# Performance work log

Measured on AMD Instinct MI355X. Metric: run time of the kernel, lower is better.

The kernel has to match this reference:

```python
import jax, jax.numpy as jnp
import numpy as np

N_NODES = 10000
N_EDGES = 80000
IN_DIM, HID, OUT_DIM, HEADS = 768, 512, 768, 4
NEG_SLOPE = 0.2


def setup_inputs() -> dict:
    key = jax.random.key(0)
    ks = jax.random.split(key, 10)
    g = 0.05
    return {
        "x": jax.random.normal(ks[0], (N_NODES, IN_DIM), jnp.float32),
        "edge_index": jax.random.randint(ks[1], (2, N_EDGES), 0, N_NODES, jnp.int64),
        # layer 1: GATConv(768 -> 512, heads=4, concat=True)
        "W1": jax.random.normal(ks[2], (IN_DIM, HEADS * HID), jnp.float32) * g,
        "a1_src": jax.random.normal(ks[3], (HEADS, HID), jnp.float32) * g,
        "a1_dst": jax.random.normal(ks[4], (HEADS, HID), jnp.float32) * g,
        "b1": jnp.zeros((HEADS * HID,), jnp.float32),
        # layer 2: GATConv(2048 -> 768, heads=1, concat=False)
        "W2": jax.random.normal(ks[5], (HEADS * HID, OUT_DIM), jnp.float32) * g,
        "a2_src": jax.random.normal(ks[6], (1, OUT_DIM), jnp.float32) * g,
        "a2_dst": jax.random.normal(ks[7], (1, OUT_DIM), jnp.float32) * g,
        "b2": jnp.zeros((OUT_DIM,), jnp.float32),
    }


def _gat_layer(x, src, dst, W, a_src, a_dst, b, heads, d_out, concat):
    N = x.shape[0]
    h = (x @ W).reshape(N, heads, d_out)              # [N, H, D]
    as_n = jnp.einsum('nhd,hd->nh', h, a_src)          # [N, H]
    ad_n = jnp.einsum('nhd,hd->nh', h, a_dst)
    e = jax.nn.leaky_relu(as_n[src] + ad_n[dst], NEG_SLOPE)  # [E, H]
    # segment softmax over destination nodes
    e_max = jax.lax.stop_gradient(jax.ops.segment_max(e, dst, num_segments=N))
    ex = jnp.exp(e - e_max[dst])
    denom = jax.ops.segment_sum(ex, dst, num_segments=N)
    alpha = ex / (denom[dst] + 1e-16)                  # [E, H]
    msg = alpha[:, :, None] * h[src]                   # [E, H, D]
    out = jax.ops.segment_sum(msg, dst, num_segments=N)  # [N, H, D]
    out = out.reshape(N, heads * d_out) if concat else out.mean(axis=1)
    return out + b


def reference(x, edge_index, W1, a1_src, a1_dst, b1, W2, a2_src, a2_dst, b2):
    N = x.shape[0]
    # PyG GATConv default: add self-loops
    loops = jnp.arange(N, dtype=edge_index.dtype)
    src = jnp.concatenate([edge_index[0], loops])
    dst = jnp.concatenate([edge_index[1], loops])
    h = _gat_layer(x, src, dst, W1, a1_src, a1_dst, b1, HEADS, HID, True)
    h = jax.nn.elu(h)
    out = _gat_layer(h, src, dst, W2, a2_src, a2_dst, b2, 1, OUT_DIM, False)
    return out
```

## Files before the change

### kernel.cpp

```cpp
#include <hip/hip_runtime.h>
#include <hip/hip_bf16.h>

#define N_NODES 10000
#define E_REAL  80000
#define E_TOTAL 90000
#define IN_DIM  768
#define HID     512
#define HEADS   4
#define OUT_DIM 768
#define HD1     (HEADS * HID)
#define NEG_SLOPE 0.2f
#define H1_HSTRIDE (N_NODES * HID)

typedef unsigned short ushort_t;
typedef unsigned int uint_t;

__device__ inline float b2f(ushort_t u) { return __uint_as_float(((uint_t)u) << 16); }
__device__ inline ushort_t f2b(float f) {
    __hip_bfloat16 h = __float2bfloat16(f);
    return *reinterpret_cast<ushort_t*>(&h);
}

__device__ inline void edge_sd(const int* __restrict__ ei, int e, int& s, int& d) {
    if (e < E_REAL) { s = ei[e]; d = ei[E_REAL + e]; }
    else            { s = e - E_REAL; d = s; }
}

#define GLDS(g, l) __builtin_amdgcn_global_load_lds( \
    (const __attribute__((address_space(1))) void*)(g), \
    (__attribute__((address_space(3))) void*)(l), 16, 0, 0)

static const long B_H1B  = 0L;
static const long B_HB   = 40960000L;
static const long B_XB   = 81920000L;
static const long B_W1T  = 97280000L;
static const long B_W2T  = 100425728L;
static const long B_SM   = 103571456L;
static const long SM_AS1   = 0;
static const long SM_AD1   = 40000;
static const long SM_AS2   = 80000;
static const long SM_AD2   = 90000;
static const long SM_CNT   = 100000;
static const long SM_ROWS  = 110000;
static const long SM_CURS  = 120016;
static const long SM_END   = 130016;
static const long B_CSRS = B_SM + SM_END * 4;

__global__ __launch_bounds__(256)
void cast_bf16(const float* __restrict__ in, ushort_t* __restrict__ o, long n) {
    long i = ((long)blockIdx.x * 256 + threadIdx.x) * 8;
    if (i >= n) return;
    float4 v0 = *(const float4*)(in + i);
    float4 v1 = *(const float4*)(in + i + 4);
    ushort_t r[8] = {f2b(v0.x), f2b(v0.y), f2b(v0.z), f2b(v0.w),
                     f2b(v1.x), f2b(v1.y), f2b(v1.z), f2b(v1.w)};
    *(uint4*)(o + i) = *(uint4*)r;
}

__global__ __launch_bounds__(256)
void cast_transpose(const float* __restrict__ W, ushort_t* __restrict__ WT,
                    int K, int N) {
    __shared__ ushort_t t[32][33];
    const int n0 = blockIdx.x * 32, k0 = blockIdx.y * 32;
    const int tx = threadIdx.x & 31, ty = threadIdx.x >> 5;
#pragma unroll
    for (int i = 0; i < 4; ++i) {
        int k = ty + i * 8;
        t[k][tx] = f2b(W[(long)(k0 + k) * N + n0 + tx]);
    }
    __syncthreads();
#pragma unroll
    for (int i = 0; i < 4; ++i) {
        int n = ty + i * 8;
        WT[(long)(n0 + n) * K + k0 + tx] = t[tx][n];
    }
}

typedef short bf16x8 __attribute__((ext_vector_type(8)));
typedef float f32x4 __attribute__((ext_vector_type(4)));

#define BM 128
#define BN 128
#define BK 32

template<int CMODE>
__global__ __launch_bounds__(256)
void gemm_bf16(const ushort_t* __restrict__ A, const ushort_t* __restrict__ BT,
               ushort_t* __restrict__ C, int M, int N, int K) {
    __shared__ ushort_t As[BM * BK];
    __shared__ ushort_t Bs[BN * BK];
    const int tid  = threadIdx.x;
    const int wave = tid >> 6, lane = tid & 63;
    const int quad = lane >> 4, l16 = lane & 15;
    const int bm = blockIdx.y * BM, bn = blockIdx.x * BN;
    const int wr = (wave >> 1) * 64, wc = (wave & 1) * 64;

    const int ch0 = wave * 128 + lane;
    const int ch1 = ch0 + 64;
    const int r0 = ch0 >> 2, c0 = (ch0 & 3) ^ ((r0 >> 1) & 3);
    const int r1 = ch1 >> 2, c1 = (ch1 & 3) ^ ((r1 >> 1) & 3);
    const ushort_t* a0 = A + (long)(bm + r0) * K + c0 * 8;
    const ushort_t* a1 = A + (long)(bm + r1) * K + c1 * 8;
    const ushort_t* b0 = BT + (long)(bn + r0) * K + c0 * 8;
    const ushort_t* b1 = BT + (long)(bn + r1) * K + c1 * 8;
    ushort_t* lA0 = As + (wave * 128) * 8;
    ushort_t* lA1 = As + (wave * 128 + 64) * 8;
    ushort_t* lB0 = Bs + (wave * 128) * 8;
    ushort_t* lB1 = Bs + (wave * 128 + 64) * 8;

    const int swz = (l16 >> 1) & 3;
    f32x4 acc[4][4] = {};

    for (int k0 = 0; k0 < K; k0 += BK) {
        GLDS(a0 + k0, lA0);
        GLDS(a1 + k0, lA1);
        GLDS(b0 + k0, lB0);
        GLDS(b1 + k0, lB1);
        __syncthreads();
        bf16x8 af[4], bfr[4];
#pragma unroll
        for (int i = 0; i < 4; ++i) {
            af[i]  = *(const bf16x8*)(As + ((wr + i * 16 + l16) * 4 + (quad ^ swz)) * 8);
            bfr[i] = *(const bf16x8*)(Bs + ((wc + i * 16 + l16) * 4 + (quad ^ swz)) * 8);
        }
#pragma unroll
        for (int i = 0; i < 4; ++i)
#pragma unroll
            for (int j = 0; j < 4; ++j)
                acc[i][j] = __builtin_amdgcn_mfma_f32_16x16x32_bf16(
                    af[i], bfr[j], acc[i][j], 0, 0, 0);
        __syncthreads();
    }

#pragma unroll
    for (int i = 0; i < 4; ++i) {
#pragma unroll
        for (int r = 0; r < 4; ++r) {
            int row = bm + wr + i * 16 + quad * 4 + r;
            if (row >= M) continue;
#pragma unroll
            for (int j = 0; j < 4; ++j) {
                int col = bn + wc + j * 16 + l16;
                if (CMODE == 0) {
                    C[(long)row * N + col] = f2b(acc[i][j][r]);
                } else {
                    C[(long)(col >> 9) * H1_HSTRIDE + (long)row * HID + (col & 511)]
                        = f2b(acc[i][j][r]);
                }
            }
        }
    }
}

__global__ __launch_bounds__(256)
void attn1(const ushort_t* __restrict__ h, const float* __restrict__ a_s,
           const float* __restrict__ a_d, float* __restrict__ os,
           float* __restrict__ od) {
    const int n = blockIdx.x;
    const int w = threadIdx.x >> 6, lane = threadIdx.x & 63;
    uint4 hv = *(const uint4*)(h + (long)w * H1_HSTRIDE + (long)n * HID + lane * 8);
    const float* asp = a_s + w * HID + lane * 8;
    const float* adp = a_d + w * HID + lane * 8;
    const ushort_t* pb = (const ushort_t*)&hv;
    float ps = 0.f, pd = 0.f;
#pragma unroll
    for (int c = 0; c < 8; ++c) {
        float v = b2f(pb[c]);
        ps += v * asp[c];
        pd += v * adp[c];
    }
#pragma unroll
    for (int off = 32; off > 0; off >>= 1) {
        ps += __shfl_down(ps, off);
        pd += __shfl_down(pd, off);
    }
    if (lane == 0) { os[n * HEADS + w] = ps; od[n * HEADS + w] = pd; }
}

__global__ __launch_bounds__(256)
void attn2(const ushort_t* __restrict__ h, const float* __restrict__ a_s,
           const float* __restrict__ a_d, float* __restrict__ os,
           float* __restrict__ od) {
    __shared__ float rs[4], rd[4];
    const int n = blockIdx.x, tid = threadIdx.x;
    const int w = tid >> 6, lane = tid & 63;
    float ps = 0.f, pd = 0.f;
#pragma unroll
    for (int j = 0; j < 3; ++j) {
        int c = tid + j * 256;
        float v = b2f(h[(long)n * OUT_DIM + c]);
        ps += v * a_s[c];
        pd += v * a_d[c];
    }
#pragma unroll
    for (int off = 32; off > 0; off >>= 1) {
        ps += __shfl_down(ps, off);
        pd += __shfl_down(pd, off);
    }
    if (lane == 0) { rs[w] = ps; rd[w] = pd; }
    __syncthreads();
    if (tid == 0) {
        os[n] = rs[0] + rs[1] + rs[2] + rs[3];
        od[n] = rd[0] + rd[1] + rd[2] + rd[3];
    }
}

__global__ __launch_bounds__(256)
void hist_dst(const int* __restrict__ ei, int* __restrict__ cnt) {
    int e = blockIdx.x * 256 + threadIdx.x;
    if (e >= E_TOTAL) return;
    int s, d; edge_sd(ei, e, s, d);
    atomicAdd(&cnt[d], 1);
}

#define SCAN_CH 40
__global__ __launch_bounds__(256)
void scan_nodes(const int* __restrict__ cnt, int* __restrict__ rows,
                int* __restrict__ curs) {
    __shared__ int part[256];
    const int tid = threadIdx.x;
    const int base = tid * SCAN_CH;
    int local[SCAN_CH];
    int sum = 0;
#pragma unroll
    for (int i = 0; i < SCAN_CH; ++i) {
        int idx = base + i;
        int v = (idx < N_NODES) ? cnt[idx] : 0;
        local[i] = v; sum += v;
    }
    part[tid] = sum;
    __syncthreads();
    for (int off = 1; off < 256; off <<= 1) {
        int v = (tid >= off) ? part[tid - off] : 0;
        __syncthreads();
        part[tid] += v;
        __syncthreads();
    }
    int run = part[tid] - sum;
#pragma unroll
    for (int i = 0; i < SCAN_CH; ++i) {
        int idx = base + i;
        if (idx < N_NODES) { rows[idx] = run; curs[idx] = run; run += local[i]; }
    }
    if (tid == 255) rows[N_NODES] = run;
}

__global__ __launch_bounds__(256)
void scatter_edges(const int* __restrict__ ei, int* __restrict__ curs,
                   int* __restrict__ csr_src) {
    int e = blockIdx.x * 256 + threadIdx.x;
    if (e >= E_TOTAL) return;
    int s, d; edge_sd(ei, e, s, d);
    int pos = atomicAdd(&curs[d], 1);
    csr_src[pos] = s;
}

__global__ __launch_bounds__(64)
void agg1(const int* __restrict__ rows, const int* __restrict__ csr_src,
          const float* __restrict__ as_n, const float* __restrict__ ad_n,
          const ushort_t* __restrict__ hf, const float* __restrict__ b1,
          ushort_t* __restrict__ o) {
    const int n = blockIdx.x, hh = blockIdx.y, lane = threadIdx.x;
    const int beg = rows[n], end = rows[n + 1];
    const ushort_t* hsl = hf + (long)hh * H1_HSTRIDE;
    const float adv = ad_n[(long)n * HEADS + hh];
    float acc[8] = {};
    float dsum = 0.f;
    for (int k = beg; k < end; k += 4) {
        int nk = end - k; if (nk > 4) nk = 4;
        uint4 v[4]; float ex[4];
#pragma unroll
        for (int u = 0; u < 4; ++u) {
            if (u < nk) {
                int s = csr_src[k + u];
                float sc = as_n[(long)s * HEADS + hh] + adv;
                sc = sc > 0.f ? sc : NEG_SLOPE * sc;
                ex[u] = __expf(sc);
                v[u]  = *(const uint4*)(hsl + (long)s * HID + lane * 8);
            }
        }
#pragma unroll
        for (int u = 0; u < 4; ++u) {
            if (u < nk) {
                dsum += ex[u];
                const ushort_t* p = (const ushort_t*)&v[u];
#pragma unroll
                for (int c = 0; c < 8; ++c) acc[c] += ex[u] * b2f(p[c]);
            }
        }
    }
    const float dinv = 1.f / (dsum + 1e-16f);
    const float* bp = b1 + hh * HID + lane * 8;
    ushort_t r[8];
#pragma unroll
    for (int c = 0; c < 8; ++c) {
        float vv = acc[c] * dinv + bp[c];
        r[c] = f2b(vv > 0.f ? vv : expm1f(vv));
    }
    *(uint4*)(o + (long)n * HD1 + hh * HID + lane * 8) = *(uint4*)r;
}

__global__ __launch_bounds__(64)
void agg2(const int* __restrict__ rows, const int* __restrict__ csr_src,
          const float* __restrict__ as_n, const float* __restrict__ ad_n,
          const ushort_t* __restrict__ hf, const float* __restrict__ b2,
          float* __restrict__ out) {
    const int n = blockIdx.x, lane = threadIdx.x;
    const int beg = rows[n], end = rows[n + 1];
    const float adv = ad_n[n];
    float acc[12] = {};
    float dsum = 0.f;
    for (int k = beg; k < end; k += 4) {
        int nk = end - k; if (nk > 4) nk = 4;
        uint4 v4[4]; uint2 v2[4]; float ex[4];
#pragma unroll
        for (int u = 0; u < 4; ++u) {
            if (u < nk) {
                int s = csr_src[k + u];
                float sc = as_n[s] + adv;
                sc = sc > 0.f ? sc : NEG_SLOPE * sc;
                ex[u] = __expf(sc);
                const ushort_t* hp = hf + (long)s * OUT_DIM;
                v4[u] = *(const uint4*)(hp + lane * 8);
                v2[u] = *(const uint2*)(hp + 512 + lane * 4);
            }
        }
#pragma unroll
        for (int u = 0; u < 4; ++u) {
            if (u < nk) {
                dsum += ex[u];
                const ushort_t* p4 = (const ushort_t*)&v4[u];
                const ushort_t* p2 = (const ushort_t*)&v2[u];
#pragma unroll
                for (int c = 0; c < 8; ++c) acc[c] += ex[u] * b2f(p4[c]);
#pragma unroll
                for (int c = 0; c < 4; ++c) acc[8 + c] += ex[u] * b2f(p2[c]);
            }
        }
    }
    const float dinv = 1.f / (dsum + 1e-16f);
    float* op = out + (long)n * OUT_DIM;
#pragma unroll
    for (int c = 0; c < 8; ++c)
        op[lane * 8 + c] = acc[c] * dinv + b2[lane * 8 + c];
#pragma unroll
    for (int c = 0; c < 4; ++c)
        op[512 + lane * 4 + c] = acc[8 + c] * dinv + b2[512 + lane * 4 + c];
}

extern "C" void kernel_launch(void* const* d_in, const int* in_sizes, int n_in,
                              void* d_out, int out_size, void* d_ws, size_t ws_size,
                              hipStream_t stream) {
    const float* x   = (const float*)d_in[0];
    const int*   ei  = (const int*)d_in[1];
    const float* W1  = (const float*)d_in[2];
    const float* a1s = (const float*)d_in[3];
    const float* a1d = (const float*)d_in[4];
    const float* b1  = (const float*)d_in[5];
    const float* W2  = (const float*)d_in[6];
    const float* a2s = (const float*)d_in[7];
    const float* a2d = (const float*)d_in[8];
    const float* b2  = (const float*)d_in[9];
    float* out = (float*)d_out;
    char* base = (char*)d_ws;

    ushort_t* h1b = (ushort_t*)(base + B_H1B);
    ushort_t* hb  = (ushort_t*)(base + B_HB);
    ushort_t* xb  = (ushort_t*)(base + B_XB);
    ushort_t* h2b = xb;
    ushort_t* w1t = (ushort_t*)(base + B_W1T);
    ushort_t* w2t = (ushort_t*)(base + B_W2T);
    float*    sm  = (float*)(base + B_SM);

    float* as1  = sm + SM_AS1;
    float* ad1  = sm + SM_AD1;
    float* as2  = sm + SM_AS2;
    float* ad2  = sm + SM_AD2;
    int* cnt    = (int*)(sm + SM_CNT);
    int* rows   = (int*)(sm + SM_ROWS);
    int* curs   = (int*)(sm + SM_CURS);
    int* csr_src = (int*)(base + B_CSRS);

    hipMemsetAsync(cnt, 0, 10000 * sizeof(int), stream);

    {
        long nx = (long)N_NODES * IN_DIM;
        cast_bf16<<<(int)(nx / 8 / 256 + 1), 256, 0, stream>>>(x, xb, nx);
        cast_transpose<<<dim3(HD1 / 32, IN_DIM / 32), 256, 0, stream>>>(W1, w1t, IN_DIM, HD1);
        cast_transpose<<<dim3(OUT_DIM / 32, HD1 / 32), 256, 0, stream>>>(W2, w2t, HD1, OUT_DIM);
        hist_dst<<<(E_TOTAL + 255) / 256, 256, 0, stream>>>(ei, cnt);
        scan_nodes<<<1, 256, 0, stream>>>(cnt, rows, curs);
        scatter_edges<<<(E_TOTAL + 255) / 256, 256, 0, stream>>>(ei, curs, csr_src);
    }

    gemm_bf16<1><<<dim3(HD1 / BN, (N_NODES + BM - 1) / BM), 256, 0, stream>>>(
        xb, w1t, h1b, N_NODES, HD1, IN_DIM);
    attn1<<<N_NODES, 256, 0, stream>>>(h1b, a1s, a1d, as1, ad1);
    agg1<<<dim3(N_NODES, HEADS), 64, 0, stream>>>(
        rows, csr_src, as1, ad1, h1b, b1, hb);

    gemm_bf16<0><<<dim3(OUT_DIM / BN, (N_NODES + BM - 1) / BM), 256, 0, stream>>>(
        hb, w2t, h2b, N_NODES, OUT_DIM, HD1);
    attn2<<<N_NODES, 256, 0, stream>>>(h2b, a2s, a2d, as2, ad2);
    agg2<<<N_NODES, 64, 0, stream>>>(
        rows, csr_src, as2, ad2, h2b, b2, out);
}
```

Measured before the change: 346.3 us.

## Replace bf16 GEMM with 8-wave 256x128x64 triple-buffered pipelined kernel

Both dense projections now use a new GEMM with 512 threads, a larger 256x128 output tile and a 64-deep K step. Operand tiles are triple-buffered in about 144KB of dynamic LDS, with global-to-LDS loads staged two iterations ahead. Explicit vmcnt waits, barriers, sched_barrier and setprio interleave the loads with the MFMA work. The aim is to hide memory latency and improve data reuse, at the cost of lower occupancy. The second GEMM also launches fewer blocks than there are CUs.

```diff
diff --git a/kernel.cpp b/kernel.cpp
--- a/kernel.cpp
+++ b/kernel.cpp
@@ -79,57 +79,125 @@
 typedef short bf16x8 __attribute__((ext_vector_type(8)));
 typedef float f32x4 __attribute__((ext_vector_type(4)));
 
-#define BM 128
-#define BN 128
-#define BK 32
+#define GBM 256
+#define GBN 128
+#define GBK 64
+#define ABUF (GBM * GBK)
+#define BBUF (GBN * GBK)
+#define GEMM_LDS_BYTES ((3 * (ABUF + BBUF)) * 2)
 
 template<int CMODE>
-__global__ __launch_bounds__(256)
-void gemm_bf16(const ushort_t* __restrict__ A, const ushort_t* __restrict__ BT,
-               ushort_t* __restrict__ C, int M, int N, int K) {
-    __shared__ ushort_t As[BM * BK];
-    __shared__ ushort_t Bs[BN * BK];
+__global__ __launch_bounds__(512)
+void gemm8p(const ushort_t* __restrict__ A, const ushort_t* __restrict__ BT,
+            ushort_t* __restrict__ C, int M, int N, int K) {
+    extern __shared__ ushort_t sm_[];
+    ushort_t* smA = sm_;
+    ushort_t* smB = sm_ + 3 * ABUF;
     const int tid  = threadIdx.x;
     const int wave = tid >> 6, lane = tid & 63;
     const int quad = lane >> 4, l16 = lane & 15;
-    const int bm = blockIdx.y * BM, bn = blockIdx.x * BN;
+    const int bm = blockIdx.y * GBM, bn = blockIdx.x * GBN;
     const int wr = (wave >> 1) * 64, wc = (wave & 1) * 64;
-
-    const int ch0 = wave * 128 + lane;
-    const int ch1 = ch0 + 64;
-    const int r0 = ch0 >> 2, c0 = (ch0 & 3) ^ ((r0 >> 1) & 3);
-    const int r1 = ch1 >> 2, c1 = (ch1 & 3) ^ ((r1 >> 1) & 3);
-    const ushort_t* a0 = A + (long)(bm + r0) * K + c0 * 8;
-    const ushort_t* a1 = A + (long)(bm + r1) * K + c1 * 8;
-    const ushort_t* b0 = BT + (long)(bn + r0) * K + c0 * 8;
-    const ushort_t* b1 = BT + (long)(bn + r1) * K + c1 * 8;
-    ushort_t* lA0 = As + (wave * 128) * 8;
-    ushort_t* lA1 = As + (wave * 128 + 64) * 8;
-    ushort_t* lB0 = Bs + (wave * 128) * 8;
-    ushort_t* lB1 = Bs + (wave * 128 + 64) * 8;
-
-    const int swz = (l16 >> 1) & 3;
+    const int NT = K / GBK;
+
+    const int  rA  = tid >> 3;
+    const long cs8 = (long)(((tid & 7) ^ ((tid >> 3) & 7)) * 8);
+    const ushort_t* aSrc = A  + (long)(bm + rA) * K + cs8;
+    const ushort_t* bSrc = BT + (long)(bn + rA) * K + cs8;
+
+    const int aRd  = (wr + l16) * GBK;
+    const int bRd  = (wc + l16) * GBK;
+    const int swz8 = l16 & 7;
+    const int chq0 = ((quad)     ^ swz8) * 8;
+    const int chq1 = ((4 + quad) ^ swz8) * 8;
+
     f32x4 acc[4][4] = {};
 
-    for (int k0 = 0; k0 < K; k0 += BK) {
-        GLDS(a0 + k0, lA0);
-        GLDS(a1 + k0, lA1);
-        GLDS(b0 + k0, lB0);
-        GLDS(b1 + k0, lB1);
-        __syncthreads();
-        bf16x8 af[4], bfr[4];
-#pragma unroll
-        for (int i = 0; i < 4; ++i) {
-            af[i]  = *(const bf16x8*)(As + ((wr + i * 16 + l16) * 4 + (quad ^ swz)) * 8);
-            bfr[i] = *(const bf16x8*)(Bs + ((wc + i * 16 + l16) * 4 + (quad ^ swz)) * 8);
-        }
+#pragma unroll
+    for (int tt = 0; tt < 2; ++tt) {
+        const long kt = (long)tt * GBK;
 #pragma unroll
         for (int i = 0; i < 4; ++i)
-#pragma unroll
-            for (int j = 0; j < 4; ++j)
-                acc[i][j] = __builtin_amdgcn_mfma_f32_16x16x32_bf16(
-                    af[i], bfr[j], acc[i][j], 0, 0, 0);
-        __syncthreads();
+            GLDS(aSrc + (long)i * 64 * K + kt,
+                 smA + tt * ABUF + (i * 512 + wave * 64) * 8);
+#pragma unroll
+        for (int i = 0; i < 2; ++i)
+            GLDS(bSrc + (long)i * 64 * K + kt,
+                 smB + tt * BBUF + (i * 512 + wave * 64) * 8);
+    }
+    asm volatile("s_waitcnt vmcnt(6)" ::: "memory");
+    __builtin_amdgcn_s_barrier();
+    __builtin_amdgcn_sched_barrier(0);
+
+    int bc = 0, bnx = 1, bs = 2;
+    for (int t = 0; t < NT; ++t) {
+        const int offA = bc * ABUF, offB = bc * BBUF;
+        const bool stage = (t + 2 < NT);
+        const long kt2 = (long)(t + 2) * GBK;
+        bf16x8 bfr[2][4], af[2][2];
+
+#pragma unroll
+        for (int j = 0; j < 4; ++j) {
+            bfr[0][j] = *(const bf16x8*)(smB + offB + bRd + j * 1024 + chq0);
+            bfr[1][j] = *(const bf16x8*)(smB + offB + bRd + j * 1024 + chq1);
+        }
+#pragma unroll
+        for (int ii = 0; ii < 2; ++ii) {
+            af[0][ii] = *(const bf16x8*)(smA + offA + aRd + ii * 1024 + chq0);
+            af[1][ii] = *(const bf16x8*)(smA + offA + aRd + ii * 1024 + chq1);
+        }
+        if (stage) {
+            GLDS(aSrc + kt2,                    smA + bs * ABUF + (wave * 64) * 8);
+            GLDS(aSrc + (long)1 * 64 * K + kt2, smA + bs * ABUF + (512 + wave * 64) * 8);
+            GLDS(aSrc + (long)2 * 64 * K + kt2, smA + bs * ABUF + (1024 + wave * 64) * 8);
+        }
+        __builtin_amdgcn_sched_barrier(0);
+        __builtin_amdgcn_s_barrier();
+        __builtin_amdgcn_sched_barrier(0);
+        __builtin_amdgcn_s_setprio(1);
+#pragma unroll
+        for (int kk = 0; kk < 2; ++kk)
+#pragma unroll
+            for (int ii = 0; ii < 2; ++ii)
+#pragma unroll
+                for (int j = 0; j < 4; ++j)
+                    acc[ii][j] = __builtin_amdgcn_mfma_f32_16x16x32_bf16(
+                        af[kk][ii], bfr[kk][j], acc[ii][j], 0, 0, 0);
+        __builtin_amdgcn_s_setprio(0);
+        __builtin_amdgcn_sched_barrier(0);
+        __builtin_amdgcn_s_barrier();
+        __builtin_amdgcn_sched_barrier(0);
+
+#pragma unroll
+        for (int ii = 0; ii < 2; ++ii) {
+            af[0][ii] = *(const bf16x8*)(smA + offA + aRd + (2 + ii) * 1024 + chq0);
+            af[1][ii] = *(const bf16x8*)(smA + offA + aRd + (2 + ii) * 1024 + chq1);
+        }
+        if (stage) {
+            GLDS(aSrc + (long)3 * 64 * K + kt2, smA + bs * ABUF + (1536 + wave * 64) * 8);
+            GLDS(bSrc + kt2,                    smB + bs * BBUF + (wave * 64) * 8);
+            GLDS(bSrc + (long)1 * 64 * K + kt2, smB + bs * BBUF + (512 + wave * 64) * 8);
+        }
+        if (stage)             { asm volatile("s_waitcnt vmcnt(6)" ::: "memory"); }
+        else if (t + 1 < NT)   { asm volatile("s_waitcnt vmcnt(0)" ::: "memory"); }
+        __builtin_amdgcn_sched_barrier(0);
+        __builtin_amdgcn_s_barrier();
+        __builtin_amdgcn_sched_barrier(0);
+        __builtin_amdgcn_s_setprio(1);
+#pragma unroll
+        for (int kk = 0; kk < 2; ++kk)
+#pragma unroll
+            for (int ii = 0; ii < 2; ++ii)
+#pragma unroll
+                for (int j = 0; j < 4; ++j)
+                    acc[2 + ii][j] = __builtin_amdgcn_mfma_f32_16x16x32_bf16(
+                        af[kk][ii], bfr[kk][j], acc[2 + ii][j], 0, 0, 0);
+        __builtin_amdgcn_s_setprio(0);
+        __builtin_amdgcn_sched_barrier(0);
+        __builtin_amdgcn_s_barrier();
+        __builtin_amdgcn_sched_barrier(0);
+
+        int tmp = bc; bc = bnx; bnx = bs; bs = tmp;
     }
 
 #pragma unroll
@@ -393,13 +461,13 @@
         scatter_edges<<<(E_TOTAL + 255) / 256, 256, 0, stream>>>(ei, curs, csr_src);
     }
 
-    gemm_bf16<1><<<dim3(HD1 / BN, (N_NODES + BM - 1) / BM), 256, 0, stream>>>(
+    gemm8p<1><<<dim3(HD1 / GBN, (N_NODES + GBM - 1) / GBM), 512, GEMM_LDS_BYTES, stream>>>(
         xb, w1t, h1b, N_NODES, HD1, IN_DIM);
     attn1<<<N_NODES, 256, 0, stream>>>(h1b, a1s, a1d, as1, ad1);
     agg1<<<dim3(N_NODES, HEADS), 64, 0, stream>>>(
         rows, csr_src, as1, ad1, h1b, b1, hb);
 
-    gemm_bf16<0><<<dim3(OUT_DIM / BN, (N_NODES + BM - 1) / BM), 256, 0, stream>>>(
+    gemm8p<0><<<dim3(OUT_DIM / GBN, (N_NODES + GBM - 1) / GBM), 512, GEMM_LDS_BYTES, stream>>>(
         hb, w2t, h2b, N_NODES, OUT_DIM, HD1);
     attn2<<<N_NODES, 256, 0, stream>>>(h2b, a2s, a2d, as2, ad2);
     agg2<<<N_NODES, 64, 0, stream>>>(
```

New measurement: 330.6 us. 1.05x faster.
